# Performance work log

Measured on AMD Instinct MI355X. Metric: run time of the kernel, lower is better.

The kernel has to match this reference:

```python
import jax, jax.numpy as jnp
import numpy as np

N_ATOMS = 500_000
N_MOLS = 25_000
HID = 300
CONSTRAINT = 0.0  # per-molecule target total (e.g. neutral net charge)
W_SCALE = 0.05    # keep random-init activations tame


def setup_inputs() -> dict:
    key = jax.random.key(0)
    ks = jax.random.split(key, 6)
    hidden = jax.random.normal(ks[0], (N_ATOMS, HID), dtype=jnp.float32)
    seg_ids = jnp.sort(jax.random.randint(ks[1], (N_ATOMS,), 0, N_MOLS, dtype=jnp.int32))
    # output readout FFN: Linear(300->300) -> ReLU -> Linear(300->1)
    W1 = jax.random.normal(ks[2], (HID, HID), dtype=jnp.float32) * W_SCALE
    b1 = jnp.zeros((HID,), dtype=jnp.float32)
    W2 = jax.random.normal(ks[3], (HID, 1), dtype=jnp.float32) * W_SCALE
    b2 = jnp.zeros((1,), dtype=jnp.float32)
    # weights readout FFN (same architecture); bias=1 keeps segment weight sums positive
    V1 = jax.random.normal(ks[4], (HID, HID), dtype=jnp.float32) * W_SCALE
    vb1 = jnp.zeros((HID,), dtype=jnp.float32)
    V2 = jax.random.normal(ks[5], (HID, 1), dtype=jnp.float32) * W_SCALE
    vb2 = jnp.ones((1,), dtype=jnp.float32)
    return {"hidden": hidden, "seg_ids": seg_ids, "W1": W1, "b1": b1, "W2": W2,
            "b2": b2, "V1": V1, "vb1": vb1, "V2": V2, "vb2": vb2}


def _ffn(x, Wa, ba, Wb, bb):
    # dropout is identity in eval mode
    h = jax.nn.relu(x @ Wa + ba)
    return h @ Wb + bb  # [N, 1]


def reference(hidden, seg_ids, W1, b1, W2, b2, V1, vb1, V2, vb2):
    output = _ffn(hidden, W1, b1, W2, b2)    # [N, 1] raw per-atom predictions
    weights = _ffn(hidden, V1, vb1, V2, vb2) # [N, 1] per-atom correction weights
    # per-molecule segment sums (replaces the Python loop over a_scope)
    sum_o = jax.ops.segment_sum(output[:, 0], seg_ids, num_segments=N_MOLS)   # [M]
    sum_w = jax.ops.segment_sum(weights[:, 0], seg_ids, num_segments=N_MOLS)  # [M]
    sum_w = jnp.where(sum_w == 0, 1.0, sum_w)  # empty segments are skipped in the original
    corr = (CONSTRAINT - sum_o) / sum_w        # [M]
    out = output + weights * corr[seg_ids][:, None]  # [N, 1]
    return out
```

## Files before the change

### kernel.cpp

```cpp
#include <hip/hip_runtime.h>
#include <stdint.h>

#define N_ATOMS 500000
#define N_MOLS  25000
#define HID     300
#define BA      64
#define WS_ELE  102400
#define NCH     19
#define SLAB    20480

typedef __attribute__((ext_vector_type(8)))  short          short8v;
typedef __attribute__((ext_vector_type(16))) float          f32x16;

static __device__ __forceinline__ unsigned short f2bf(float f) {
  unsigned int u = __float_as_uint(f);
  u += 0x7fffu + ((u >> 16) & 1u);
  return (unsigned short)(u >> 16);
}

static __device__ __forceinline__ short8v pack8(float4 a, float4 b) {
  short8v r;
  r[0] = (short)f2bf(a.x); r[1] = (short)f2bf(a.y);
  r[2] = (short)f2bf(a.z); r[3] = (short)f2bf(a.w);
  r[4] = (short)f2bf(b.x); r[5] = (short)f2bf(b.y);
  r[6] = (short)f2bf(b.z); r[7] = (short)f2bf(b.w);
  return r;
}

static __device__ __forceinline__ void loadA(const float* hp, int k0,
                                             float4& f0, float4& f1) {
  if (k0 <= 288) {
    f0 = *reinterpret_cast<const float4*>(hp + k0);
    f1 = *reinterpret_cast<const float4*>(hp + k0 + 4);
  } else {
    f0 = *reinterpret_cast<const float4*>(hp + 296);
    f1 = make_float4(0.f, 0.f, 0.f, 0.f);
  }
}

static __device__ __forceinline__ void stage16(const char* gsrc, char* ldst, int ln) {
  __builtin_amdgcn_global_load_lds(
      (const __attribute__((address_space(1))) void*)(gsrc + ln * 16),
      (__attribute__((address_space(3))) void*)ldst, 16, 0, 0);
}

__global__ void prep_kernel(
    const float* __restrict__ W1, const float* __restrict__ V1,
    const float* __restrict__ b1, const float* __restrict__ vb1,
    const float* __restrict__ W2, const float* __restrict__ V2,
    unsigned short* __restrict__ W1s, unsigned short* __restrict__ V1s,
    float* __restrict__ b1p, float* __restrict__ vb1p,
    float* __restrict__ W2p, float* __restrict__ V2p,
    float* __restrict__ sums)
{
  const int t = blockIdx.x * 256 + threadIdx.x;
  if (t < 2 * WS_ELE) {
    const float* src = (t < WS_ELE) ? W1 : V1;
    unsigned short* dst = (t < WS_ELE) ? W1s : V1s;
    const int i    = (t < WS_ELE) ? t : t - WS_ELE;
    const int j    = i & 7;
    const int lane = (i >> 3) & 63;
    const int nt   = (i >> 9) % 10;
    const int kc16 = i / 5120;
    const int k = kc16 * 16 + (lane >> 5) * 8 + j;
    const int n = nt * 32 + (lane & 31);
    const float v = (k < HID && n < HID) ? src[k * HID + n] : 0.f;
    dst[i] = f2bf(v);
  } else if (t < 2 * WS_ELE + 1280) {
    const int i = t - 2 * WS_ELE;
    const int which = i / 320;
    const int e = i - which * 320;
    const float* s = (which == 0) ? b1 : (which == 1) ? vb1 : (which == 2) ? W2 : V2;
    float*       d = (which == 0) ? b1p : (which == 1) ? vb1p : (which == 2) ? W2p : V2p;
    d[e] = (e < HID) ? s[e] : 0.f;
  } else if (t < 2 * WS_ELE + 1280 + 2 * N_MOLS) {
    sums[t - (2 * WS_ELE + 1280)] = 0.f;
  }
}

__global__ __launch_bounds__(512, 4) void fused_ffn(
    const float* __restrict__ hidden,
    const unsigned short* __restrict__ W1s, const unsigned short* __restrict__ V1s,
    const float* __restrict__ b1p, const float* __restrict__ vb1p,
    const float* __restrict__ W2p, const float* __restrict__ V2p,
    const float* __restrict__ b2, const float* __restrict__ vb2,
    float* __restrict__ outA, float* __restrict__ outW)
{
  __shared__ char lds[2 * SLAB];
  __shared__ float sOutA[BA];
  __shared__ float sOutW[BA];

  const int tid = (int)threadIdx.x;
  const int ln  = tid & 63;
  const int wv  = tid >> 6;
  const int mtx = wv & 1;
  const int ch  = (wv >> 1) & 1;
  const int rg  = wv >> 2;
  const int l31 = ln & 31;
  const int lh  = ln >> 5;
  const long base = (long)blockIdx.x * BA;

  long rowl = base + rg * 32 + l31;
  if (rowl > N_ATOMS - 1) rowl = N_ATOMS - 1;
  const float* hp = hidden + rowl * (long)HID;

  const int p0 = (wv < 4) ? wv * 3 : 12 + (wv - 4) * 2;
  const int np = (wv < 4) ? 3 : 2;

  f32x16 acc[5] = {};

  float4 c0, c1;
  loadA(hp, lh * 8, c0, c1);
  #pragma unroll
  for (int r = 0; r < 3; ++r) {
    if (r < np) {
      const int c = p0 + r;
      const char* src = (c < 10) ? ((const char*)W1s + c * 1024)
                                 : ((const char*)V1s + (c - 10) * 1024);
      stage16(src, lds + c * 1024, ln);
    }
  }
  __syncthreads();

  for (int c = 0; c < NCH; ++c) {
    const char* buf = lds + (c & 1) * SLAB;

    float4 n0, n1;
    if (c < NCH - 1) {
      loadA(hp, (c + 1) * 16 + lh * 8, n0, n1);
      char* nbuf = lds + ((c + 1) & 1) * SLAB;
      const char* wsrc = (const char*)W1s + (c + 1) * 10240;
      const char* vsrc = (const char*)V1s + (c + 1) * 10240;
      #pragma unroll
      for (int r = 0; r < 3; ++r) {
        if (r < np) {
          const int cc = p0 + r;
          const char* src = (cc < 10) ? (wsrc + cc * 1024) : (vsrc + (cc - 10) * 1024);
          stage16(src, nbuf + cc * 1024, ln);
        }
      }
    }

    const short8v af = pack8(c0, c1);
    const char* bb = buf + mtx * 10240 + ch * 5120;
    #pragma unroll
    for (int nt = 0; nt < 5; ++nt) {
      const short8v bf = *reinterpret_cast<const short8v*>(bb + nt * 1024 + ln * 16);
      acc[nt] = __builtin_amdgcn_mfma_f32_32x32x16_bf16(af, bf, acc[nt], 0, 0, 0);
    }

    if (c < NCH - 1) { c0 = n0; c1 = n1; }
    __syncthreads();
  }

  float bv[5], w2[5];
  const float* bbv = mtx ? vb1p : b1p;
  const float* ww2 = mtx ? V2p  : W2p;
  #pragma unroll
  for (int nt = 0; nt < 5; ++nt) {
    const int cix = ch * 160 + nt * 32 + l31;
    bv[nt] = bbv[cix];
    w2[nt] = ww2[cix];
  }
  if (tid < BA) { sOutA[tid] = 0.f; sOutW[tid] = 0.f; }
  __syncthreads();

  float* sOut = mtx ? sOutW : sOutA;
  #pragma unroll
  for (int r = 0; r < 16; ++r) {
    float s = 0.f;
    #pragma unroll
    for (int nt = 0; nt < 5; ++nt) {
      float x = fmaxf(acc[nt][r] + bv[nt], 0.f);
      s = fmaf(x, w2[nt], s);
    }
    s += __shfl_xor(s, 1);
    s += __shfl_xor(s, 2);
    s += __shfl_xor(s, 4);
    s += __shfl_xor(s, 8);
    s += __shfl_xor(s, 16);
    if (l31 == 0) {
      const int row = rg * 32 + (r & 3) + 8 * (r >> 2) + 4 * lh;
      atomicAdd(&sOut[row], s);
    }
  }
  __syncthreads();
  if (tid < BA) {
    const long atom = base + tid;
    if (atom < N_ATOMS) {
      outA[atom] = sOutA[tid] + b2[0];
      outW[atom] = sOutW[tid] + vb2[0];
    }
  }
}

__global__ void segsum_kernel(
    const float* __restrict__ outA, const float* __restrict__ outW,
    const int* __restrict__ seg,
    float* __restrict__ sum_o, float* __restrict__ sum_w)
{
  const long i0 = ((long)blockIdx.x * 256 + threadIdx.x) * 8;
  if (i0 >= N_ATOMS) return;
  const int4   s0 = *reinterpret_cast<const int4*>(seg + i0);
  const int4   s1 = *reinterpret_cast<const int4*>(seg + i0 + 4);
  const float4 o0 = *reinterpret_cast<const float4*>(outA + i0);
  const float4 o1 = *reinterpret_cast<const float4*>(outA + i0 + 4);
  const float4 w0 = *reinterpret_cast<const float4*>(outW + i0);
  const float4 w1 = *reinterpret_cast<const float4*>(outW + i0 + 4);
  const int   ss[8] = {s0.x, s0.y, s0.z, s0.w, s1.x, s1.y, s1.z, s1.w};
  const float oo[8] = {o0.x, o0.y, o0.z, o0.w, o1.x, o1.y, o1.z, o1.w};
  const float ww[8] = {w0.x, w0.y, w0.z, w0.w, w1.x, w1.y, w1.z, w1.w};
  int cur = ss[0];
  float ao = 0.f, aw = 0.f;
  #pragma unroll
  for (int j = 0; j < 8; ++j) {
    if (ss[j] != cur) {
      atomicAdd(&sum_o[cur], ao);
      atomicAdd(&sum_w[cur], aw);
      cur = ss[j]; ao = 0.f; aw = 0.f;
    }
    ao += oo[j]; aw += ww[j];
  }
  atomicAdd(&sum_o[cur], ao);
  atomicAdd(&sum_w[cur], aw);
}

__global__ void final_kernel(
    const float* __restrict__ outA, const float* __restrict__ outW,
    const int* __restrict__ seg,
    const float* __restrict__ sum_o, const float* __restrict__ sum_w,
    float* __restrict__ out)
{
  const long i0 = ((long)blockIdx.x * 256 + threadIdx.x) * 4;
  if (i0 >= N_ATOMS) return;
  const int4   s4 = *reinterpret_cast<const int4*>(seg + i0);
  const float4 o4 = *reinterpret_cast<const float4*>(outA + i0);
  const float4 w4 = *reinterpret_cast<const float4*>(outW + i0);
  const int   ss[4] = {s4.x, s4.y, s4.z, s4.w};
  const float oo[4] = {o4.x, o4.y, o4.z, o4.w};
  const float ww[4] = {w4.x, w4.y, w4.z, w4.w};
  float r[4];
  #pragma unroll
  for (int j = 0; j < 4; ++j) {
    const int s = ss[j];
    float sw = sum_w[s];
    sw = (sw == 0.f) ? 1.f : sw;
    const float corr = (0.f - sum_o[s]) / sw;
    r[j] = oo[j] + ww[j] * corr;
  }
  *reinterpret_cast<float4*>(out + i0) = make_float4(r[0], r[1], r[2], r[3]);
}

extern "C" void kernel_launch(void* const* d_in, const int* in_sizes, int n_in,
                              void* d_out, int out_size, void* d_ws, size_t ws_size,
                              hipStream_t stream)
{
  const float* hidden = (const float*)d_in[0];
  const int*   seg    = (const int*)d_in[1];
  const float* W1     = (const float*)d_in[2];
  const float* b1     = (const float*)d_in[3];
  const float* W2     = (const float*)d_in[4];
  const float* b2     = (const float*)d_in[5];
  const float* V1     = (const float*)d_in[6];
  const float* vb1    = (const float*)d_in[7];
  const float* V2     = (const float*)d_in[8];
  const float* vb2    = (const float*)d_in[9];

  char* ws = (char*)d_ws;
  float*          outA  = (float*)(ws + 0);
  float*          outW  = (float*)(ws + 2000000);
  float*          sum_o = (float*)(ws + 4000000);
  float*          sum_w = (float*)(ws + 4100000);
  unsigned short* W1s   = (unsigned short*)(ws + 4200000);
  unsigned short* V1s   = (unsigned short*)(ws + 4404800);
  float*          b1p   = (float*)(ws + 4609600);
  float*          vb1p  = (float*)(ws + 4610880);
  float*          W2p   = (float*)(ws + 4612160);
  float*          V2p   = (float*)(ws + 4613440);

  prep_kernel<<<1001, 256, 0, stream>>>(W1, V1, b1, vb1, W2, V2,
                                        W1s, V1s, b1p, vb1p, W2p, V2p, sum_o);

  const int nblk = (N_ATOMS + BA - 1) / BA;
  fused_ffn<<<nblk, 512, 0, stream>>>(hidden, W1s, V1s, b1p, vb1p, W2p, V2p,
                                      b2, vb2, outA, outW);

  segsum_kernel<<<(N_ATOMS / 8 + 255) / 256, 256, 0, stream>>>(outA, outW, seg,
                                                               sum_o, sum_w);

  final_kernel<<<(N_ATOMS / 4 + 255) / 256, 256, 0, stream>>>(outA, outW, seg,
                                                              sum_o, sum_w,
                                                              (float*)d_out);
}
```

Baseline: 474.4 us.

## Triple-buffer weight staging with manual vmcnt waits and a single barrier per chunk

Moves the K-loop from double to triple-buffered LDS staging of the bf16 W1/V1 slabs and prefetches the hidden-row fragments two chunks ahead. Explicit s_waitcnt vmcnt counts plus one s_barrier per iteration replace the trailing __syncthreads, so loads can overlap the MFMAs more deeply. It also drops the bounds branch in loadA, which now reads past column 300 into the next row (and slightly past the buffer end on the last row), and uses the HIP bf16 conversion intrinsic. The LDS footprint rises to about 60 KB per block, which may cut the number of resident blocks per CU below what the launch bounds request.

```diff
diff --git a/kernel.cpp b/kernel.cpp
--- a/kernel.cpp
+++ b/kernel.cpp
@@ -1,4 +1,5 @@
 #include <hip/hip_runtime.h>
+#include <hip/hip_bf16.h>
 #include <stdint.h>
 
 #define N_ATOMS 500000
@@ -19,23 +20,18 @@
 }
 
 static __device__ __forceinline__ short8v pack8(float4 a, float4 b) {
-  short8v r;
-  r[0] = (short)f2bf(a.x); r[1] = (short)f2bf(a.y);
-  r[2] = (short)f2bf(a.z); r[3] = (short)f2bf(a.w);
-  r[4] = (short)f2bf(b.x); r[5] = (short)f2bf(b.y);
-  r[6] = (short)f2bf(b.z); r[7] = (short)f2bf(b.w);
-  return r;
+  union { __hip_bfloat16 h[8]; short8v v; } u;
+  u.h[0] = __float2bfloat16(a.x); u.h[1] = __float2bfloat16(a.y);
+  u.h[2] = __float2bfloat16(a.z); u.h[3] = __float2bfloat16(a.w);
+  u.h[4] = __float2bfloat16(b.x); u.h[5] = __float2bfloat16(b.y);
+  u.h[6] = __float2bfloat16(b.z); u.h[7] = __float2bfloat16(b.w);
+  return u.v;
 }
 
 static __device__ __forceinline__ void loadA(const float* hp, int k0,
                                              float4& f0, float4& f1) {
-  if (k0 <= 288) {
-    f0 = *reinterpret_cast<const float4*>(hp + k0);
-    f1 = *reinterpret_cast<const float4*>(hp + k0 + 4);
-  } else {
-    f0 = *reinterpret_cast<const float4*>(hp + 296);
-    f1 = make_float4(0.f, 0.f, 0.f, 0.f);
-  }
+  f0 = *reinterpret_cast<const float4*>(hp + k0);
+  f1 = *reinterpret_cast<const float4*>(hp + k0 + 4);
 }
 
 static __device__ __forceinline__ void stage16(const char* gsrc, char* ldst, int ln) {
@@ -86,7 +82,7 @@
     const float* __restrict__ b2, const float* __restrict__ vb2,
     float* __restrict__ outA, float* __restrict__ outW)
 {
-  __shared__ char lds[2 * SLAB];
+  __shared__ char lds[3 * SLAB];
   __shared__ float sOutA[BA];
   __shared__ float sOutW[BA];
 
@@ -107,51 +103,70 @@
   const int p0 = (wv < 4) ? wv * 3 : 12 + (wv - 4) * 2;
   const int np = (wv < 4) ? 3 : 2;
 
+#define STAGE(slabIdx, dstbuf) do {                                            \
+    const char* wsrc_ = (const char*)W1s + (slabIdx) * 10240;                  \
+    const char* vsrc_ = (const char*)V1s + (slabIdx) * 10240;                  \
+    _Pragma("unroll")                                                          \
+    for (int r_ = 0; r_ < 3; ++r_) {                                           \
+      if (r_ < np) {                                                           \
+        const int cc_ = p0 + r_;                                               \
+        const char* src_ = (cc_ < 10) ? (wsrc_ + cc_ * 1024)                   \
+                                      : (vsrc_ + (cc_ - 10) * 1024);           \
+        stage16(src_, (dstbuf) + cc_ * 1024, ln);                              \
+      }                                                                        \
+    }                                                                          \
+  } while (0)
+
+#define COMPUTE(bufptr, A0, A1) do {                                           \
+    const short8v af_ = pack8(A0, A1);                                         \
+    const char* bb_ = (bufptr) + mtx * 10240 + ch * 5120;                      \
+    _Pragma("unroll")                                                          \
+    for (int nt_ = 0; nt_ < 5; ++nt_) {                                        \
+      const short8v bf_ = *reinterpret_cast<const short8v*>(                   \
+          bb_ + nt_ * 1024 + ln * 16);                                         \
+      acc[nt_] = __builtin_amdgcn_mfma_f32_32x32x16_bf16(af_, bf_, acc[nt_], 0, 0, 0); \
+    }                                                                          \
+  } while (0)
+
   f32x16 acc[5] = {};
-
-  float4 c0, c1;
-  loadA(hp, lh * 8, c0, c1);
-  #pragma unroll
-  for (int r = 0; r < 3; ++r) {
-    if (r < np) {
-      const int c = p0 + r;
-      const char* src = (c < 10) ? ((const char*)W1s + c * 1024)
-                                 : ((const char*)V1s + (c - 10) * 1024);
-      stage16(src, lds + c * 1024, ln);
-    }
-  }
-  __syncthreads();
-
-  for (int c = 0; c < NCH; ++c) {
-    const char* buf = lds + (c & 1) * SLAB;
-
-    float4 n0, n1;
-    if (c < NCH - 1) {
-      loadA(hp, (c + 1) * 16 + lh * 8, n0, n1);
-      char* nbuf = lds + ((c + 1) & 1) * SLAB;
-      const char* wsrc = (const char*)W1s + (c + 1) * 10240;
-      const char* vsrc = (const char*)V1s + (c + 1) * 10240;
-      #pragma unroll
-      for (int r = 0; r < 3; ++r) {
-        if (r < np) {
-          const int cc = p0 + r;
-          const char* src = (cc < 10) ? (wsrc + cc * 1024) : (vsrc + (cc - 10) * 1024);
-          stage16(src, nbuf + cc * 1024, ln);
-        }
-      }
-    }
-
-    const short8v af = pack8(c0, c1);
-    const char* bb = buf + mtx * 10240 + ch * 5120;
-    #pragma unroll
-    for (int nt = 0; nt < 5; ++nt) {
-      const short8v bf = *reinterpret_cast<const short8v*>(bb + nt * 1024 + ln * 16);
-      acc[nt] = __builtin_amdgcn_mfma_f32_32x32x16_bf16(af, bf, acc[nt], 0, 0, 0);
-    }
-
-    if (c < NCH - 1) { c0 = n0; c1 = n1; }
-    __syncthreads();
-  }
+  float4 cA0, cA1, nA0, nA1;
+
+  loadA(hp, lh * 8, cA0, cA1);
+  STAGE(0, lds + 0 * SLAB);
+  loadA(hp, 16 + lh * 8, nA0, nA1);
+  STAGE(1, lds + 1 * SLAB);
+
+  int ic = 0, i2 = 2;
+  for (int c = 0; c < NCH - 2; ++c) {
+    float4 fA0, fA1;
+    loadA(hp, (c + 2) * 16 + lh * 8, fA0, fA1);
+    __builtin_amdgcn_sched_barrier(0);
+    if (wv < 4) asm volatile("s_waitcnt vmcnt(7)" ::: "memory");
+    else        asm volatile("s_waitcnt vmcnt(6)" ::: "memory");
+    __builtin_amdgcn_s_barrier();
+    __builtin_amdgcn_sched_barrier(0);
+    STAGE(c + 2, lds + i2 * SLAB);
+    COMPUTE(lds + ic * SLAB, cA0, cA1);
+    cA0 = nA0; cA1 = nA1; nA0 = fA0; nA1 = fA1;
+    ic = (ic == 2) ? 0 : ic + 1;
+    i2 = (i2 == 2) ? 0 : i2 + 1;
+  }
+  __builtin_amdgcn_sched_barrier(0);
+  if (wv < 4) asm volatile("s_waitcnt vmcnt(5)" ::: "memory");
+  else        asm volatile("s_waitcnt vmcnt(4)" ::: "memory");
+  __builtin_amdgcn_s_barrier();
+  __builtin_amdgcn_sched_barrier(0);
+  COMPUTE(lds + ic * SLAB, cA0, cA1);
+  cA0 = nA0; cA1 = nA1;
+  ic = (ic == 2) ? 0 : ic + 1;
+  __builtin_amdgcn_sched_barrier(0);
+  asm volatile("s_waitcnt vmcnt(0)" ::: "memory");
+  __builtin_amdgcn_s_barrier();
+  __builtin_amdgcn_sched_barrier(0);
+  COMPUTE(lds + ic * SLAB, cA0, cA1);
+
+#undef STAGE
+#undef COMPUTE
 
   float bv[5], w2[5];
   const float* bbv = mtx ? vb1p : b1p;
```

Result: slower. 523.3 us (+10.3%).
